# Optimization experiments

Hardware: AMD Instinct MI355X
Metric: run time of the kernel (lower is better)

Reference implementation:

```python
import jax, jax.numpy as jnp
import numpy as np

D_MODEL = 768
N_HEADS = 12
HEAD = D_MODEL // N_HEADS  # 64


def setup_inputs() -> dict:
    key = jax.random.key(0)
    ks = jax.random.split(key, 10)
    s = 1.0 / np.sqrt(D_MODEL)
    x = jax.random.normal(ks[0], (4, 2048, D_MODEL), dtype=jnp.float32)
    # per-head projection weights stacked: [H, D, head]
    Wq = jax.random.normal(ks[1], (N_HEADS, D_MODEL, HEAD), dtype=jnp.float32) * s
    bq = jax.random.normal(ks[2], (N_HEADS, HEAD), dtype=jnp.float32) * 0.01
    Wk = jax.random.normal(ks[3], (N_HEADS, D_MODEL, HEAD), dtype=jnp.float32) * s
    bk = jax.random.normal(ks[4], (N_HEADS, HEAD), dtype=jnp.float32) * 0.01
    Wv = jax.random.normal(ks[5], (N_HEADS, D_MODEL, HEAD), dtype=jnp.float32) * s
    bv = jax.random.normal(ks[6], (N_HEADS, HEAD), dtype=jnp.float32) * 0.01
    Wo = jax.random.normal(ks[7], (D_MODEL, D_MODEL), dtype=jnp.float32) * s
    bo = jax.random.normal(ks[8], (D_MODEL,), dtype=jnp.float32) * 0.01
    return {"x": x, "Wq": Wq, "bq": bq, "Wk": Wk, "bk": bk,
            "Wv": Wv, "bv": bv, "Wo": Wo, "bo": bo}


def reference(x, Wq, bq, Wk, bk, Wv, bv, Wo, bo):
    # x: [B,S,D]; per-head projections fused over the head axis.
    q = jnp.einsum('bsd,hde->bhse', x, Wq) + bq[None, :, None, :]
    k = jnp.einsum('bsd,hde->bhse', x, Wk) + bk[None, :, None, :]
    v = jnp.einsum('bsd,hde->bhse', x, Wv) + bv[None, :, None, :]
    scale = 1.0 / jnp.sqrt(jnp.asarray(HEAD, dtype=x.dtype))
    scores = jnp.einsum('bhqe,bhke->bhqk', q, k) * scale  # [B,H,S,S]
    attn = jax.nn.softmax(scores, axis=-1)
    out = jnp.einsum('bhqk,bhke->bhqe', attn, v)  # [B,H,S,head]
    B, H, S, E = out.shape
    # concat heads (head order 0..H-1 along last dim)
    out = out.transpose(0, 2, 1, 3).reshape(B, S, H * E)
    return out @ Wo + bo
```

## Files before the change

### kernel.cpp

```cpp
#include <hip/hip_runtime.h>

typedef __bf16 bf16x8 __attribute__((ext_vector_type(8)));
typedef __bf16 bf16x4 __attribute__((ext_vector_type(4)));
typedef float f32x4 __attribute__((ext_vector_type(4)));

#define QSCALE 0.18033688011112042f

__device__ __forceinline__ void gload16(const void* g, void* l) {
  __builtin_amdgcn_global_load_lds((const __attribute__((address_space(1))) void*)g,
                                   (__attribute__((address_space(3))) void*)l, 16, 0, 0);
}

__device__ __forceinline__ float fexp2(float x) {
#if __has_builtin(__builtin_amdgcn_exp2f)
  return __builtin_amdgcn_exp2f(x);
#else
  return exp2f(x);
#endif
}

__device__ __forceinline__ f32x4 mfma16(bf16x8 a, bf16x8 b, f32x4 c) {
  return __builtin_amdgcn_mfma_f32_16x16x32_bf16(a, b, c, 0, 0, 0);
}

__device__ __forceinline__ unsigned pkbf(float a, float b) {
  union { __bf16 h[2]; unsigned u; } t;
  t.h[0] = (__bf16)a; t.h[1] = (__bf16)b;
  return t.u;
}

__device__ __forceinline__ void pl16swap(unsigned& a, unsigned& b, int g) {
#if __has_builtin(__builtin_amdgcn_permlane16_swap)
  auto r = __builtin_amdgcn_permlane16_swap(a, b, false, false);
  a = r[0]; b = r[1];
#else
  unsigned as_ = (unsigned)__shfl_xor((int)a, 16, 64);
  unsigned bs_ = (unsigned)__shfl_xor((int)b, 16, 64);
  bool odd = g & 1;
  unsigned an = odd ? bs_ : a;
  unsigned bn = odd ? b : as_;
  a = an; b = bn;
#endif
}

__global__ __launch_bounds__(256) void k_cvt_x(const float4* __restrict__ x,
                                               bf16x4* __restrict__ xb) {
  int i = blockIdx.x * 256 + threadIdx.x;
  float4 v = x[i];
  bf16x4 o;
  o[0] = (__bf16)v.x; o[1] = (__bf16)v.y; o[2] = (__bf16)v.z; o[3] = (__bf16)v.w;
  xb[i] = o;
}

__global__ __launch_bounds__(256) void k_cvt_wqkv(
    const float* __restrict__ Wq, const float* __restrict__ Wk,
    const float* __restrict__ Wv, const float* __restrict__ bq,
    const float* __restrict__ bk, const float* __restrict__ bv,
    __bf16* __restrict__ Wt, float* __restrict__ bias) {
  int g = blockIdx.x * 256 + threadIdx.x;
  int n = g / 192;
  int d4 = g - n * 192;
  int d = d4 * 4;
  int t = n / 768;
  int rr = n - t * 768;
  int h = rr >> 6, e = rr & 63;
  const float* W = (t == 0) ? Wq : ((t == 1) ? Wk : Wv);
  const float* bs = (t == 0) ? bq : ((t == 1) ? bk : bv);
  bf16x4 o;
#pragma unroll
  for (int i = 0; i < 4; ++i) o[i] = (__bf16)W[(size_t)(h * 768 + d + i) * 64 + e];
  *(bf16x4*)(Wt + (size_t)n * 768 + d) = o;
  if (d4 == 0) bias[n] = bs[h * 64 + e];
}

__global__ __launch_bounds__(256) void k_cvt_wo(const float* __restrict__ Wo,
                                                __bf16* __restrict__ Wt) {
  int g = blockIdx.x * 256 + threadIdx.x;
  int n = g / 192;
  int d4 = g - n * 192;
  int d = d4 * 4;
  bf16x4 o;
#pragma unroll
  for (int i = 0; i < 4; ++i) o[i] = (__bf16)Wo[(size_t)(d + i) * 768 + n];
  *(bf16x4*)(Wt + (size_t)n * 768 + d) = o;
}

template <int MODE>
__global__ __launch_bounds__(256, 2) void k_gemm(
    const __bf16* __restrict__ A, const __bf16* __restrict__ Bt,
    const float* __restrict__ bias, __bf16* __restrict__ Qd,
    __bf16* __restrict__ Kd, __bf16* __restrict__ VTd,
    float* __restrict__ outF) {
  constexpr int KD = 768;
  __shared__ __bf16 As[2][128 * 64];
  __shared__ __bf16 Bs[2][128 * 64];
  const int tid = threadIdx.x, lane = tid & 63, wid = tid >> 6;
  const int wr = wid >> 1, wc = wid & 1;
  const int bm = blockIdx.x, bn = blockIdx.y;
  const f32x4 z4 = {0.f, 0.f, 0.f, 0.f};
  f32x4 acc[4][4];
#pragma unroll
  for (int a = 0; a < 4; ++a)
#pragma unroll
    for (int b = 0; b < 4; ++b) acc[a][b] = z4;

  const char* Ab = (const char*)A + (size_t)bm * 128 * (KD * 2);
  const char* Bb = (const char*)Bt + (size_t)bn * 128 * (KD * 2);

  auto stage = [&](int kb, int buf) {
#pragma unroll
    for (int i = 0; i < 4; ++i) {
      int o = (wid * 4 + i) * 1024 + lane * 16;
      int row = o >> 7;
      int col = (o & 127) ^ ((row & 7) << 4);
      gload16(Ab + (size_t)row * (KD * 2) + kb * 128 + col,
              (char*)As[buf] + (wid * 4 + i) * 1024);
      gload16(Bb + (size_t)row * (KD * 2) + kb * 128 + col,
              (char*)Bs[buf] + (wid * 4 + i) * 1024);
    }
  };

  stage(0, 0);

  for (int kb = 0; kb < KD / 64; ++kb) {
    const int cur = kb & 1;
    if (kb < KD / 64 - 1) {
      stage(kb + 1, cur ^ 1);
      asm volatile("s_waitcnt vmcnt(8)" ::: "memory");
    } else {
      asm volatile("s_waitcnt vmcnt(0)" ::: "memory");
    }
    __builtin_amdgcn_s_barrier();
#pragma unroll
    for (int ks = 0; ks < 2; ++ks) {
      bf16x8 af[4], bfr[4];
#pragma unroll
      for (int ar = 0; ar < 4; ++ar) {
        int rl = wr * 64 + ar * 16 + (lane & 15);
        int byt = rl * 128 + ((ks * 64 + (lane >> 4) * 16) ^ ((rl & 7) << 4));
        af[ar] = *(const bf16x8*)((const char*)As[cur] + byt);
      }
#pragma unroll
      for (int bc = 0; bc < 4; ++bc) {
        int rl = wc * 64 + bc * 16 + (lane & 15);
        int byt = rl * 128 + ((ks * 64 + (lane >> 4) * 16) ^ ((rl & 7) << 4));
        bfr[bc] = *(const bf16x8*)((const char*)Bs[cur] + byt);
      }
#pragma unroll
      for (int ar = 0; ar < 4; ++ar)
#pragma unroll
        for (int bc = 0; bc < 4; ++bc)
          acc[ar][bc] = mfma16(af[ar], bfr[bc], acc[ar][bc]);
    }
    __builtin_amdgcn_s_barrier();
  }

#pragma unroll
  for (int ar = 0; ar < 4; ++ar) {
#pragma unroll
    for (int bc = 0; bc < 4; ++bc) {
      int n = bn * 128 + wc * 64 + bc * 16 + (lane & 15);
      float bval = bias[n];
#pragma unroll
      for (int r = 0; r < 4; ++r) {
        int m = bm * 128 + wr * 64 + ar * 16 + (lane >> 4) * 4 + r;
        float val = acc[ar][bc][r] + bval;
        if constexpr (MODE == 0) {
          int t = n / 768;
          int rr = n - t * 768;
          int h = rr >> 6, e = rr & 63;
          int b = m >> 11, s = m & 2047;
          size_t bh = (size_t)(b * 12 + h);
          if (t == 0)
            Qd[(bh * 2048 + s) * 64 + e] = (__bf16)(val * QSCALE);
          else if (t == 1)
            Kd[(bh * 2048 + s) * 64 + e] = (__bf16)val;
          else
            VTd[(bh * 64 + e) * 2048 + s] = (__bf16)val;
        } else {
          outF[(size_t)m * 768 + n] = val;
        }
      }
    }
  }
}

__global__ __launch_bounds__(256, 3) void k_attn(const __bf16* __restrict__ Qg,
                                                 const __bf16* __restrict__ Kg,
                                                 const __bf16* __restrict__ Vg,
                                                 __bf16* __restrict__ AO) {
  constexpr int S = 2048;
  __shared__ __bf16 Ks[2][64 * 64];
  __shared__ __bf16 Vs[2][64 * 64];
  const int tid = threadIdx.x, lane = tid & 63, wid = tid >> 6;
  const int q = lane & 15, g = lane >> 4;
  const int q7s = (q & 7) << 4;
  const int vg = ((g & 1) << 5) | ((g >> 1) << 4);
  const int lin = blockIdx.x + blockIdx.y * 16;
  const int xcd = lin & 7, pos = lin >> 3;
  const int bh = xcd * 6 + (pos >> 4);
  const int qt = pos & 15;
  const int bb = bh / 12, hh = bh - bb * 12;
  const size_t hoff = (size_t)bh * S * 64;
  const int q0 = qt * 128 + wid * 32;

  bf16x8 qb[2][2];
#pragma unroll
  for (int rt = 0; rt < 2; ++rt)
#pragma unroll
    for (int ks = 0; ks < 2; ++ks)
      qb[rt][ks] = *(const bf16x8*)(Qg + hoff + (size_t)(q0 + rt * 16 + q) * 64 +
                                    ks * 32 + g * 8);

  const f32x4 z4 = {0.f, 0.f, 0.f, 0.f};
  f32x4 acc[2][4];
#pragma unroll
  for (int a = 0; a < 2; ++a)
#pragma unroll
    for (int b = 0; b < 4; ++b) acc[a][b] = z4;
  float l_p[2] = {0.f, 0.f};

  const char* Kb = (const char*)(Kg + hoff);
  const char* Vb = (const char*)(Vg + (size_t)bh * 64 * S);

  auto stage = [&](int kv, int buf) {
#pragma unroll
    for (int i = 0; i < 2; ++i) {
      int o = (wid * 2 + i) * 1024 + lane * 16;
      int row = o >> 7;
      int col = (o & 127) ^ ((row & 7) << 4);
      gload16(Kb + (size_t)(kv * 64 + row) * 128 + col,
              (char*)Ks[buf] + (wid * 2 + i) * 1024);
      gload16(Vb + (size_t)row * (S * 2) + (size_t)kv * 128 + col,
              (char*)Vs[buf] + (wid * 2 + i) * 1024);
    }
  };

  stage(0, 0);

  for (int kv = 0; kv < S / 64; ++kv) {
    const int cur = kv & 1;
    if (kv < S / 64 - 1) {
      stage(kv + 1, cur ^ 1);
      asm volatile("s_waitcnt vmcnt(4)" ::: "memory");
    } else {
      asm volatile("s_waitcnt vmcnt(0)" ::: "memory");
    }
    __builtin_amdgcn_s_barrier();
    const char* Kc = (const char*)Ks[cur];
    const char* Vc = (const char*)Vs[cur];

    f32x4 sa[4][2];
#pragma unroll
    for (int ct = 0; ct < 4; ++ct) {
      sa[ct][0] = z4;
      sa[ct][1] = z4;
    }
    __builtin_amdgcn_s_setprio(1);
#pragma unroll
    for (int ks = 0; ks < 2; ++ks)
#pragma unroll
      for (int ct = 0; ct < 4; ++ct) {
        int rl = ct * 16 + q;
        bf16x8 ka = *(const bf16x8*)(Kc + rl * 128 + ((ks * 64 + g * 16) ^ q7s));
        sa[ct][0] = mfma16(ka, qb[0][ks], sa[ct][0]);
        sa[ct][1] = mfma16(ka, qb[1][ks], sa[ct][1]);
      }
    __builtin_amdgcn_s_setprio(0);

    bf16x8 vf[2][4];
#pragma unroll
    for (int ks = 0; ks < 2; ++ks)
#pragma unroll
      for (int et = 0; et < 4; ++et) {
        int rl = et * 16 + q;
        vf[ks][et] = *(const bf16x8*)(Vc + rl * 128 + ((ks * 64 + vg) ^ q7s));
      }
    __builtin_amdgcn_s_barrier();

    bf16x8 pb[2][2];
#pragma unroll
    for (int rt = 0; rt < 2; ++rt) {
      float sum = 0.f;
      unsigned w[4][2];
#pragma unroll
      for (int ct = 0; ct < 4; ++ct) {
        float p0 = fexp2(sa[ct][rt][0]);
        float p1 = fexp2(sa[ct][rt][1]);
        float p2 = fexp2(sa[ct][rt][2]);
        float p3 = fexp2(sa[ct][rt][3]);
        sum += (p0 + p1) + (p2 + p3);
        w[ct][0] = pkbf(p0, p1);
        w[ct][1] = pkbf(p2, p3);
      }
      l_p[rt] += sum;
      pl16swap(w[0][0], w[1][0], g);
      pl16swap(w[0][1], w[1][1], g);
      pl16swap(w[2][0], w[3][0], g);
      pl16swap(w[2][1], w[3][1], g);
      union { unsigned u[4]; bf16x8 v; } f0, f1;
      f0.u[0] = w[0][0]; f0.u[1] = w[0][1]; f0.u[2] = w[1][0]; f0.u[3] = w[1][1];
      f1.u[0] = w[2][0]; f1.u[1] = w[2][1]; f1.u[2] = w[3][0]; f1.u[3] = w[3][1];
      pb[rt][0] = f0.v;
      pb[rt][1] = f1.v;
    }

    __builtin_amdgcn_s_setprio(1);
#pragma unroll
    for (int ks = 0; ks < 2; ++ks)
#pragma unroll
      for (int et = 0; et < 4; ++et) {
        acc[0][et] = mfma16(vf[ks][et], pb[0][ks], acc[0][et]);
        acc[1][et] = mfma16(vf[ks][et], pb[1][ks], acc[1][et]);
      }
    __builtin_amdgcn_s_setprio(0);
  }

#pragma unroll
  for (int rt = 0; rt < 2; ++rt) {
    float l = l_p[rt];
    l += __shfl_xor(l, 16, 64);
    l += __shfl_xor(l, 32, 64);
    float inv = 1.0f / l;
    int srow = q0 + rt * 16 + q;
#pragma unroll
    for (int et = 0; et < 4; ++et) {
      bf16x4 ov;
#pragma unroll
      for (int r = 0; r < 4; ++r) ov[r] = (__bf16)(acc[rt][et][r] * inv);
      *(bf16x4*)(AO + ((size_t)bb * S + srow) * 768 + hh * 64 + et * 16 + g * 4) =
          ov;
    }
  }
}

extern "C" void kernel_launch(void* const* d_in, const int* in_sizes, int n_in,
                              void* d_out, int out_size, void* d_ws,
                              size_t ws_size, hipStream_t stream) {
  const float* x = (const float*)d_in[0];
  const float* Wq = (const float*)d_in[1];
  const float* bq = (const float*)d_in[2];
  const float* Wk = (const float*)d_in[3];
  const float* bk = (const float*)d_in[4];
  const float* Wv = (const float*)d_in[5];
  const float* bv = (const float*)d_in[6];
  const float* Wo = (const float*)d_in[7];
  const float* bo = (const float*)d_in[8];
  float* out = (float*)d_out;
  char* ws = (char*)d_ws;

  __bf16* xb = (__bf16*)(ws + 0);
  __bf16* wqkv = (__bf16*)(ws + 12582912);
  __bf16* wot = (__bf16*)(ws + 16121856);
  float* biasq = (float*)(ws + 17301504);
  __bf16* Qb = (__bf16*)(ws + 17310720);
  __bf16* Kb = (__bf16*)(ws + 29893632);
  __bf16* VT = (__bf16*)(ws + 42476544);

  k_cvt_x<<<6144, 256, 0, stream>>>((const float4*)x, (bf16x4*)xb);
  k_cvt_wqkv<<<1728, 256, 0, stream>>>(Wq, Wk, Wv, bq, bk, bv, wqkv, biasq);
  k_cvt_wo<<<576, 256, 0, stream>>>(Wo, wot);
  k_gemm<0><<<dim3(64, 18), 256, 0, stream>>>(xb, wqkv, biasq, Qb, Kb, VT,
                                              nullptr);
  k_attn<<<dim3(16, 48), 256, 0, stream>>>(Qb, Kb, VT, xb );
  k_gemm<1><<<dim3(64, 6), 256, 0, stream>>>(xb, wot, bo, nullptr, nullptr,
                                             nullptr, out);
}
```

Measured before the change: 164.1 us.

## Merge conversion kernels into one launch and use single-barrier prefetch loops

The three fp32-to-bf16 conversion kernels are merged into one launch that dispatches on block index, removing two kernel launches. In the GEMM and attention main loops, the prefetch of the next tile now happens after a full vmcnt(0) wait and barrier, and the trailing barrier is dropped, so each iteration has one barrier instead of two. The trade-off is that the loop now waits for all outstanding loads, including the prefetch just issued in the previous iteration, rather than keeping one tile in flight. That may expose global-load latency that the older wait count hid.

```diff
diff --git a/kernel.cpp b/kernel.cpp
--- a/kernel.cpp
+++ b/kernel.cpp
@@ -43,46 +43,46 @@
 #endif
 }
 
-__global__ __launch_bounds__(256) void k_cvt_x(const float4* __restrict__ x,
-                                               bf16x4* __restrict__ xb) {
-  int i = blockIdx.x * 256 + threadIdx.x;
-  float4 v = x[i];
-  bf16x4 o;
-  o[0] = (__bf16)v.x; o[1] = (__bf16)v.y; o[2] = (__bf16)v.z; o[3] = (__bf16)v.w;
-  xb[i] = o;
-}
-
-__global__ __launch_bounds__(256) void k_cvt_wqkv(
+__global__ __launch_bounds__(256) void k_cvt_all(
+    const float4* __restrict__ x, bf16x4* __restrict__ xb,
     const float* __restrict__ Wq, const float* __restrict__ Wk,
     const float* __restrict__ Wv, const float* __restrict__ bq,
     const float* __restrict__ bk, const float* __restrict__ bv,
-    __bf16* __restrict__ Wt, float* __restrict__ bias) {
-  int g = blockIdx.x * 256 + threadIdx.x;
-  int n = g / 192;
-  int d4 = g - n * 192;
-  int d = d4 * 4;
-  int t = n / 768;
-  int rr = n - t * 768;
-  int h = rr >> 6, e = rr & 63;
-  const float* W = (t == 0) ? Wq : ((t == 1) ? Wk : Wv);
-  const float* bs = (t == 0) ? bq : ((t == 1) ? bk : bv);
-  bf16x4 o;
-#pragma unroll
-  for (int i = 0; i < 4; ++i) o[i] = (__bf16)W[(size_t)(h * 768 + d + i) * 64 + e];
-  *(bf16x4*)(Wt + (size_t)n * 768 + d) = o;
-  if (d4 == 0) bias[n] = bs[h * 64 + e];
-}
-
-__global__ __launch_bounds__(256) void k_cvt_wo(const float* __restrict__ Wo,
-                                                __bf16* __restrict__ Wt) {
-  int g = blockIdx.x * 256 + threadIdx.x;
-  int n = g / 192;
-  int d4 = g - n * 192;
-  int d = d4 * 4;
-  bf16x4 o;
-#pragma unroll
-  for (int i = 0; i < 4; ++i) o[i] = (__bf16)Wo[(size_t)(d + i) * 768 + n];
-  *(bf16x4*)(Wt + (size_t)n * 768 + d) = o;
+    __bf16* __restrict__ Wt, float* __restrict__ bias,
+    const float* __restrict__ Wo, __bf16* __restrict__ Wot) {
+  int b = blockIdx.x;
+  if (b < 6144) {
+    int i = b * 256 + threadIdx.x;
+    float4 v = x[i];
+    bf16x4 o;
+    o[0] = (__bf16)v.x; o[1] = (__bf16)v.y; o[2] = (__bf16)v.z; o[3] = (__bf16)v.w;
+    xb[i] = o;
+  } else if (b < 6144 + 1728) {
+    int g = (b - 6144) * 256 + threadIdx.x;
+    int n = g / 192;
+    int d4 = g - n * 192;
+    int d = d4 * 4;
+    int t = n / 768;
+    int rr = n - t * 768;
+    int h = rr >> 6, e = rr & 63;
+    const float* W = (t == 0) ? Wq : ((t == 1) ? Wk : Wv);
+    const float* bs = (t == 0) ? bq : ((t == 1) ? bk : bv);
+    bf16x4 o;
+#pragma unroll
+    for (int i = 0; i < 4; ++i)
+      o[i] = (__bf16)W[(size_t)(h * 768 + d + i) * 64 + e];
+    *(bf16x4*)(Wt + (size_t)n * 768 + d) = o;
+    if (d4 == 0) bias[n] = bs[h * 64 + e];
+  } else {
+    int g = (b - 6144 - 1728) * 256 + threadIdx.x;
+    int n = g / 192;
+    int d4 = g - n * 192;
+    int d = d4 * 4;
+    bf16x4 o;
+#pragma unroll
+    for (int i = 0; i < 4; ++i) o[i] = (__bf16)Wo[(size_t)(d + i) * 768 + n];
+    *(bf16x4*)(Wot + (size_t)n * 768 + d) = o;
+  }
 }
 
 template <int MODE>
@@ -124,13 +124,9 @@
 
   for (int kb = 0; kb < KD / 64; ++kb) {
     const int cur = kb & 1;
-    if (kb < KD / 64 - 1) {
-      stage(kb + 1, cur ^ 1);
-      asm volatile("s_waitcnt vmcnt(8)" ::: "memory");
-    } else {
-      asm volatile("s_waitcnt vmcnt(0)" ::: "memory");
-    }
+    asm volatile("s_waitcnt vmcnt(0)" ::: "memory");
     __builtin_amdgcn_s_barrier();
+    if (kb < KD / 64 - 1) stage(kb + 1, cur ^ 1);
 #pragma unroll
     for (int ks = 0; ks < 2; ++ks) {
       bf16x8 af[4], bfr[4];
@@ -152,7 +148,6 @@
         for (int bc = 0; bc < 4; ++bc)
           acc[ar][bc] = mfma16(af[ar], bfr[bc], acc[ar][bc]);
     }
-    __builtin_amdgcn_s_barrier();
   }
 
 #pragma unroll
@@ -240,13 +235,9 @@
 
   for (int kv = 0; kv < S / 64; ++kv) {
     const int cur = kv & 1;
-    if (kv < S / 64 - 1) {
-      stage(kv + 1, cur ^ 1);
-      asm volatile("s_waitcnt vmcnt(4)" ::: "memory");
-    } else {
-      asm volatile("s_waitcnt vmcnt(0)" ::: "memory");
-    }
+    asm volatile("s_waitcnt vmcnt(0)" ::: "memory");
     __builtin_amdgcn_s_barrier();
+    if (kv < S / 64 - 1) stage(kv + 1, cur ^ 1);
     const char* Kc = (const char*)Ks[cur];
     const char* Vc = (const char*)Vs[cur];
 
@@ -276,7 +267,6 @@
         int rl = et * 16 + q;
         vf[ks][et] = *(const bf16x8*)(Vc + rl * 128 + ((ks * 64 + vg) ^ q7s));
       }
-    __builtin_amdgcn_s_barrier();
 
     bf16x8 pb[2][2];
 #pragma unroll
@@ -357,9 +347,9 @@
   __bf16* Kb = (__bf16*)(ws + 29893632);
   __bf16* VT = (__bf16*)(ws + 42476544);
 
-  k_cvt_x<<<6144, 256, 0, stream>>>((const float4*)x, (bf16x4*)xb);
-  k_cvt_wqkv<<<1728, 256, 0, stream>>>(Wq, Wk, Wv, bq, bk, bv, wqkv, biasq);
-  k_cvt_wo<<<576, 256, 0, stream>>>(Wo, wot);
+  k_cvt_all<<<6144 + 1728 + 576, 256, 0, stream>>>(
+      (const float4*)x, (bf16x4*)xb, Wq, Wk, Wv, bq, bk, bv, wqkv, biasq, Wo,
+      wot);
   k_gemm<0><<<dim3(64, 18), 256, 0, stream>>>(xb, wqkv, biasq, Qb, Kb, VT,
                                               nullptr);
   k_attn<<<dim3(16, 48), 256, 0, stream>>>(Qb, Kb, VT, xb );
```

New measurement: 173.0 us. 1.05x slower.
